# Optimization experiments

Measured on AMD Instinct MI355X. Metric: run time of the kernel, lower is better.

## Reference

```python
import jax, jax.numpy as jnp
import numpy as np

K = 15  # window_size


def setup_inputs() -> dict:
    key = jax.random.key(0)
    k1, k2, k3, k4 = jax.random.split(key, 4)
    x = jax.random.normal(k1, (8, 256, 240, 240), dtype=jnp.float32)
    wq = jax.random.normal(k2, (144, 256), dtype=jnp.float32) * (1.0 / np.sqrt(256))
    wk = jax.random.normal(k3, (144, 256), dtype=jnp.float32) * (1.0 / np.sqrt(256))
    wproj = jax.random.normal(k4, (256, 256), dtype=jnp.float32) * (1.0 / np.sqrt(256))
    return {"x": x, "wq": wq, "wk": wk, "wproj": wproj}


def _pnlm(x, wq, wk, wproj):
    b, c, h, w = x.shape
    ph, pw = (-h) % K, (-w) % K
    if ph or pw:
        x_pad = jnp.pad(x, ((0, 0), (0, 0), (0, ph), (0, pw)), mode='reflect')
    else:
        x_pad = x
    H, W = x_pad.shape[2], x_pad.shape[3]
    nh, nw = H // K, W // K
    N = K * K  # tokens per window
    # blockify: (B,C,H,W) -> (B*nh*nw, C, N)
    blocks = (x_pad.reshape(b, c, nh, K, nw, K)
              .transpose(0, 2, 4, 1, 3, 5)
              .reshape(b * nh * nw, c, N))
    q = jnp.einsum('ec,bcn->bne', wq, blocks)   # (B', N, E)
    km = jnp.einsum('ec,bcm->bem', wk, blocks)  # (B', E, N)
    att = jnp.einsum('bne,bem->bnm', q, km)     # (B', N, N)
    scale = 1.0 / jnp.sqrt(jnp.asarray(q.shape[-1], dtype=att.dtype))
    att = jax.nn.softmax(att * scale, axis=-1)
    y = jnp.einsum('bnm,bcm->bcn', att, blocks)  # att @ V, V = blocks^T
    y = jnp.einsum('oc,bcn->bon', wproj, y)      # 1x1 proj_out
    # unblockify: (B', C, N) -> (B, C, H, W)
    y = (y.reshape(b, nh, nw, c, K, K)
         .transpose(0, 3, 1, 4, 2, 5)
         .reshape(b, c, H, W))
    y = y[:, :, :h, :w]
    return x + y


def reference(x, wq, wk, wproj):
    return _pnlm(x, wq, wk, wproj)
```

## Files before the change

kernel.cpp:

```cpp
#include <hip/hip_runtime.h>


typedef __bf16 bf16x8 __attribute__((ext_vector_type(8)));
typedef float  f32x4  __attribute__((ext_vector_type(4)));

#define MFMA(a,b,c) __builtin_amdgcn_mfma_f32_16x16x32_bf16((a),(b),(c),0,0,0)

#define QK_ROW 320
#define KL_STRIDE 168
#define XBB_ROW 240

__device__ __forceinline__ unsigned short f2bf(float f){
  union { float f; unsigned int u; } v; v.f = f;
  unsigned int r = v.u + 0x7FFFu + ((v.u >> 16) & 1u);
  return (unsigned short)(r >> 16);
}
__device__ __forceinline__ float bf2f(unsigned short u){
  union { unsigned int u; float f; } v; v.u = ((unsigned int)u) << 16;
  return v.f;
}
__device__ __forceinline__ int swz(int row, int col){
  return row*256 + ((((col >> 3) ^ (row & 7)) << 3) | (col & 7));
}
__device__ __forceinline__ bf16x8 ld_frag_lds(const unsigned short* p, int idx){
  uint4 v = *(const uint4*)(p + idx);
  return __builtin_bit_cast(bf16x8, v);
}
__device__ __forceinline__ bf16x8 ld_frag_b(const void* p){
  uint4 v = *(const uint4*)(p);
  return __builtin_bit_cast(bf16x8, v);
}

__device__ __forceinline__ void repack_frag(const unsigned int* plo, const unsigned int* phi,
                                            uint4* outf, int lane){
  const int nn = lane & 15, hh = lane >> 4;
  const int sla = nn + 32*(hh & 1);
  const int slb = sla + 16;
  const bool up = hh >= 2;
  #pragma unroll
  for (int k = 0; k < 8; ++k){
    unsigned int a0 = (unsigned int)__shfl((int)plo[2*k],   sla);
    unsigned int a1 = (unsigned int)__shfl((int)plo[2*k+1], sla);
    unsigned int b0 = (unsigned int)__shfl((int)phi[2*k],   sla);
    unsigned int b1 = (unsigned int)__shfl((int)phi[2*k+1], sla);
    unsigned int c0 = (unsigned int)__shfl((int)plo[2*k],   slb);
    unsigned int c1 = (unsigned int)__shfl((int)plo[2*k+1], slb);
    unsigned int d0 = (unsigned int)__shfl((int)phi[2*k],   slb);
    unsigned int d1 = (unsigned int)__shfl((int)phi[2*k+1], slb);
    outf[k] = make_uint4(up?a1:a0, up?b1:b0, up?c1:c0, up?d1:d0);
  }
}

__global__ __launch_bounds__(256) void k_xb(
    const float* __restrict__ x, unsigned short* __restrict__ xbb)
{
  __shared__ unsigned short xs[8*15*240];
  const int wg = blockIdx.x;
  const int cg = wg & 31;
  const int th = (wg >> 5) & 15;
  const int b  = wg >> 9;
  const int tid = threadIdx.x;

  const float* xb = x + ((size_t)b*256 + cg*8)*57600 + th*15*240;
  for (int i = tid; i < 8*15*120; i += 256){
    int c = i / 1800;
    int rem = i - c*1800;
    int r = rem / 120, p2 = rem - r*120;
    float2 v = *(const float2*)(xb + (size_t)c*57600 + r*240 + p2*2);
    *(unsigned int*)(&xs[(c*15 + r)*240 + p2*2]) =
        (unsigned int)f2bf(v.x) | ((unsigned int)f2bf(v.y) << 16);
  }
  __syncthreads();

  for (int i = tid; i < 8*16*30; i += 256){
    int c = i / 480;
    int rem = i - c*480;
    int tw = rem / 30, ch = rem - tw*30;
    union { unsigned short u16[8]; uint4 u4; } pk;
    #pragma unroll
    for (int j = 0; j < 8; ++j){
      int m = ch*8 + j;
      int r = m / 15, s = m - r*15;
      pk.u16[j] = (m <= 224) ? xs[(c*15 + r)*240 + tw*15 + s] : (unsigned short)0;
    }
    *(uint4*)(xbb + ((size_t)(b*256 + th*16 + tw)*256 + cg*8 + c)*XBB_ROW + ch*8) = pk.u4;
  }
}

__global__ __launch_bounds__(512) void k_qk(
    const float* __restrict__ x, const float* __restrict__ wq,
    const float* __restrict__ wk,
    unsigned short* __restrict__ qkws)
{
  __shared__ __align__(16) unsigned short S[32768];
  unsigned short* xt  = S;
  unsigned short* wqs = S;
  unsigned short* wks = S + 8192;
  const int wg  = blockIdx.x;
  const int b   = wg / 450;
  const int hw0 = (wg % 450) * 128;
  const int tid = threadIdx.x;
  const int lane = tid & 63, wave = tid >> 6;
  const int col  = lane & 15, hi = lane >> 4;

  {
    const float* xb = x + (size_t)b * 256 * 57600 + hw0;
    const int hw_l = tid & 127;
    #pragma unroll 4
    for (int i = 0; i < 32; ++i){
      int c = ((tid >> 7) * 32 + i) * 2;
      float f0 = xb[(size_t)c     * 57600 + hw_l];
      float f1 = xb[(size_t)(c+1) * 57600 + hw_l];
      *(unsigned int*)(&xt[swz(hw_l, c)]) =
          (unsigned int)f2bf(f0) | ((unsigned int)f2bf(f1) << 16);
    }
  }
  __syncthreads();

  bf16x8 af[8];
  const int arow = wave*16 + col;
  #pragma unroll
  for (int k = 0; k < 8; ++k)
    af[k] = ld_frag_lds(xt, swz(arow, k*32 + hi*8));

  const size_t orow_base = (size_t)b*57600 + hw0 + wave*16;

  for (int eg = 0; eg < 5; ++eg){
    __syncthreads();
    for (int i = 0; i < 8; ++i){
      int idx = tid + i*512;
      int e_l = idx >> 7, c = (idx & 127) * 2;
      int e = eg*32 + e_l;
      float2 vq = make_float2(0.f,0.f), vk = make_float2(0.f,0.f);
      if (e < 144){
        vq = *(const float2*)(wq + (size_t)e*256 + c);
        vk = *(const float2*)(wk + (size_t)e*256 + c);
      }
      *(unsigned int*)(&wqs[swz(e_l, c)]) =
          (unsigned int)f2bf(vq.x) | ((unsigned int)f2bf(vq.y) << 16);
      *(unsigned int*)(&wks[swz(e_l, c)]) =
          (unsigned int)f2bf(vk.x) | ((unsigned int)f2bf(vk.y) << 16);
    }
    __syncthreads();
    #pragma unroll
    for (int etl = 0; etl < 2; ++etl){
      f32x4 aq = {0.f,0.f,0.f,0.f}, ak = {0.f,0.f,0.f,0.f};
      const int el = etl*16 + col;
      #pragma unroll
      for (int k = 0; k < 8; ++k){
        int idx = swz(el, k*32 + hi*8);
        bf16x8 bq = ld_frag_lds(wqs, idx);
        bf16x8 bk = ld_frag_lds(wks, idx);
        aq = MFMA(af[k], bq, aq);
        ak = MFMA(af[k], bk, ak);
      }
      const int e_out = eg*32 + etl*16 + col;
      #pragma unroll
      for (int jj = 0; jj < 4; ++jj){
        size_t row = orow_base + hi*4 + jj;
        qkws[row*QK_ROW + e_out]       = f2bf(aq[jj]);
        qkws[row*QK_ROW + 160 + e_out] = f2bf(ak[jj]);
      }
    }
  }
}

__global__ __launch_bounds__(512,4) void k_attn_b(
    const unsigned short* __restrict__ xbb, const float* __restrict__ wproj,
    const unsigned short* __restrict__ qkws, float* __restrict__ out)
{
  __shared__ __align__(16) unsigned short S[40320 + 480];
  unsigned short* kl = S;
  unsigned short* xl = S;
  unsigned short* wl = S + 32768;
  unsigned int*  hwp = (unsigned int*)(S + 40320);
  const int wg = blockIdx.x;
  const int b  = wg >> 8;
  const int th = (wg >> 4) & 15, tw = wg & 15;
  const int h0 = th*15, w0 = tw*15;
  const int tid = threadIdx.x;
  const int lane = tid & 63, wave = tid >> 6;
  const int col  = lane & 15, hi = lane >> 4;
  const size_t obase = (size_t)b * 256 * 57600;
  const unsigned short* qkb = qkws + (size_t)b * 57600 * QK_ROW;
  const unsigned short* xbw = xbb + (size_t)wg * (256*XBB_ROW);

  if (tid < 240){
    int ms = tid <= 224 ? tid : 224;
    hwp[tid] = (unsigned int)((h0 + ms/15)*240 + w0 + ms%15);
  }
  __syncthreads();

  for (int i = tid; i < 240*20; i += 512){
    int m = i / 20, eb = i - m*20;
    *(uint4*)(&kl[m*KL_STRIDE + eb*8]) =
        *(const uint4*)(qkb + (size_t)hwp[m]*QK_ROW + 160 + eb*8);
  }
  __syncthreads();

  uint4 attf[2][8];
  #pragma unroll
  for (int slot = 0; slot < 2; ++slot){
    const int nt = wave + slot*8;
    if (nt < 15){
      const int n  = nt*16 + col;
      const int na = n <= 224 ? n : 224;
      const unsigned short* qrow = qkb + (size_t)hwp[na]*QK_ROW;
      bf16x8 qf[5];
      #pragma unroll
      for (int c = 0; c < 5; ++c)
        qf[c] = ld_frag_b(qrow + c*32 + hi*8);
      f32x4 at[15];
      #pragma unroll
      for (int T = 0; T < 15; ++T){
        f32x4 acc = {0.f,0.f,0.f,0.f};
        #pragma unroll
        for (int c = 0; c < 5; ++c){
          bf16x8 kf = ld_frag_lds(kl, (T*16 + col)*KL_STRIDE + c*32 + hi*8);
          acc = MFMA(kf, qf[c], acc);
        }
        at[T] = acc;
      }
      const float sc = 0.12022458674074695f;
      float M = -3.0e38f;
      #pragma unroll
      for (int T = 0; T < 15; ++T){
        #pragma unroll
        for (int jj = 0; jj < 4; ++jj){
          int m = T*16 + hi*4 + jj;
          if (m <= 224) M = fmaxf(M, at[T][jj]*sc);
        }
      }
      M = fmaxf(M, __shfl_xor(M, 16));
      M = fmaxf(M, __shfl_xor(M, 32));
      float Ssum = 0.f;
      #pragma unroll
      for (int T = 0; T < 15; ++T){
        #pragma unroll
        for (int jj = 0; jj < 4; ++jj){
          int m = T*16 + hi*4 + jj;
          float v = (m <= 224) ? exp2f(at[T][jj]*sc - M) : 0.f;
          at[T][jj] = v; Ssum += v;
        }
      }
      Ssum += __shfl_xor(Ssum, 16);
      Ssum += __shfl_xor(Ssum, 32);
      const float inv = 1.0f / Ssum;
      unsigned int plo[16], phi[16];
      #pragma unroll
      for (int T = 0; T < 15; ++T){
        plo[T] = (unsigned int)f2bf(at[T][0]*inv) | ((unsigned int)f2bf(at[T][1]*inv) << 16);
        phi[T] = (unsigned int)f2bf(at[T][2]*inv) | ((unsigned int)f2bf(at[T][3]*inv) << 16);
      }
      plo[15] = 0u; phi[15] = 0u;
      repack_frag(plo, phi, attf[slot], lane);
    }
  }

  unsigned int ylo[2][16], yhi[2][16];
  #pragma unroll
  for (int half = 0; half < 2; ++half){
    __syncthreads();
    for (int i = tid; i < 128*32; i += 512){
      int c = i >> 5, m8 = i & 31;
      uint4 v = make_uint4(0u,0u,0u,0u);
      if (m8 < 30)
        v = *(const uint4*)(xbw + (size_t)(half*128 + c)*XBB_ROW + m8*8);
      *(uint4*)(&xl[swz(c, m8*8)]) = v;
    }
    __syncthreads();
    #pragma unroll
    for (int slot = 0; slot < 2; ++slot){
      const int nt = wave + slot*8;
      if (nt < 15){
        #pragma unroll
        for (int ct = 0; ct < 8; ++ct){
          f32x4 acc = {0.f,0.f,0.f,0.f};
          #pragma unroll
          for (int k = 0; k < 8; ++k){
            bf16x8 xf = ld_frag_lds(xl, swz(ct*16 + col, k*32 + hi*8));
            acc = MFMA(xf, __builtin_bit_cast(bf16x8, attf[slot][k]), acc);
          }
          ylo[slot][half*8 + ct] = (unsigned int)f2bf(acc[0]) | ((unsigned int)f2bf(acc[1]) << 16);
          yhi[slot][half*8 + ct] = (unsigned int)f2bf(acc[2]) | ((unsigned int)f2bf(acc[3]) << 16);
        }
      }
    }
  }

  uint4 y1f[2][8];
  #pragma unroll
  for (int slot = 0; slot < 2; ++slot){
    const int nt = wave + slot*8;
    if (nt < 15)
      repack_frag(ylo[slot], yhi[slot], y1f[slot], lane);
  }

  #pragma unroll 1
  for (int oe = 0; oe < 16; ++oe){
    __syncthreads();
    for (int i = tid; i < 16*128; i += 512){
      int olr = i >> 7, c = (i & 127)*2;
      const float* wr = wproj + (size_t)(oe*16 + olr)*256 + c;
      *(unsigned int*)(&wl[swz(olr, c)]) =
          (unsigned int)f2bf(wr[0]) | ((unsigned int)f2bf(wr[1]) << 16);
    }
    __syncthreads();
    bf16x8 awf[8];
    #pragma unroll
    for (int k = 0; k < 8; ++k)
      awf[k] = ld_frag_lds(wl, swz(col, k*32 + hi*8));
    #pragma unroll
    for (int slot = 0; slot < 2; ++slot){
      const int nt = wave + slot*8;
      if (nt < 15){
        f32x4 y2 = {0.f,0.f,0.f,0.f};
        #pragma unroll
        for (int k = 0; k < 8; ++k)
          y2 = MFMA(awf[k], __builtin_bit_cast(bf16x8, y1f[slot][k]), y2);
        const int n = nt*16 + col;
        if (n <= 224){
          const size_t pix = hwp[n];
          #pragma unroll
          for (int jj = 0; jj < 4; ++jj){
            int o = oe*16 + hi*4 + jj;
            float xr = bf2f(xbw[(size_t)o*XBB_ROW + n]);
            out[obase + (size_t)o*57600 + pix] = y2[jj] + xr;
          }
        }
      }
    }
  }
}

__global__ __launch_bounds__(512,4) void k_attn_s(
    const float* __restrict__ x, const float* __restrict__ wproj,
    const unsigned short* __restrict__ qkws, float* __restrict__ out)
{
  __shared__ __align__(16) unsigned short S[40320 + 480];
  unsigned short* kl = S;
  unsigned short* xl = S;
  unsigned short* wl = S + 32768;
  unsigned int*  hwp = (unsigned int*)(S + 40320);
  const int wg = blockIdx.x;
  const int b  = wg >> 8;
  const int th = (wg >> 4) & 15, tw = wg & 15;
  const int h0 = th*15, w0 = tw*15;
  const int tid = threadIdx.x;
  const int lane = tid & 63, wave = tid >> 6;
  const int col  = lane & 15, hi = lane >> 4;
  const size_t xbase = (size_t)b * 256 * 57600;
  const unsigned short* qkb = qkws + (size_t)b * 57600 * QK_ROW;

  if (tid < 240){
    int ms = tid <= 224 ? tid : 224;
    hwp[tid] = (unsigned int)((h0 + ms/15)*240 + w0 + ms%15);
  }
  __syncthreads();

  for (int i = tid; i < 240*20; i += 512){
    int m = i / 20, eb = i - m*20;
    *(uint4*)(&kl[m*KL_STRIDE + eb*8]) =
        *(const uint4*)(qkb + (size_t)hwp[m]*QK_ROW + 160 + eb*8);
  }
  __syncthreads();

  uint4 attf[2][8];
  #pragma unroll
  for (int slot = 0; slot < 2; ++slot){
    const int nt = wave + slot*8;
    if (nt < 15){
      const int n  = nt*16 + col;
      const int na = n <= 224 ? n : 224;
      const unsigned short* qrow = qkb + (size_t)hwp[na]*QK_ROW;
      bf16x8 qf[5];
      #pragma unroll
      for (int c = 0; c < 5; ++c)
        qf[c] = ld_frag_b(qrow + c*32 + hi*8);
      f32x4 at[15];
      #pragma unroll
      for (int T = 0; T < 15; ++T){
        f32x4 acc = {0.f,0.f,0.f,0.f};
        #pragma unroll
        for (int c = 0; c < 5; ++c){
          bf16x8 kf = ld_frag_lds(kl, (T*16 + col)*KL_STRIDE + c*32 + hi*8);
          acc = MFMA(kf, qf[c], acc);
        }
        at[T] = acc;
      }
      const float sc = 0.12022458674074695f;
      float M = -3.0e38f;
      #pragma unroll
      for (int T = 0; T < 15; ++T){
        #pragma unroll
        for (int jj = 0; jj < 4; ++jj){
          int m = T*16 + hi*4 + jj;
          if (m <= 224) M = fmaxf(M, at[T][jj]*sc);
        }
      }
      M = fmaxf(M, __shfl_xor(M, 16));
      M = fmaxf(M, __shfl_xor(M, 32));
      float Ssum = 0.f;
      #pragma unroll
      for (int T = 0; T < 15; ++T){
        #pragma unroll
        for (int jj = 0; jj < 4; ++jj){
          int m = T*16 + hi*4 + jj;
          float v = (m <= 224) ? exp2f(at[T][jj]*sc - M) : 0.f;
          at[T][jj] = v; Ssum += v;
        }
      }
      Ssum += __shfl_xor(Ssum, 16);
      Ssum += __shfl_xor(Ssum, 32);
      const float inv = 1.0f / Ssum;
      unsigned int plo[16], phi[16];
      #pragma unroll
      for (int T = 0; T < 15; ++T){
        plo[T] = (unsigned int)f2bf(at[T][0]*inv) | ((unsigned int)f2bf(at[T][1]*inv) << 16);
        phi[T] = (unsigned int)f2bf(at[T][2]*inv) | ((unsigned int)f2bf(at[T][3]*inv) << 16);
      }
      plo[15] = 0u; phi[15] = 0u;
      repack_frag(plo, phi, attf[slot], lane);
    }
  }

  unsigned int ylo[2][16], yhi[2][16];
  #pragma unroll
  for (int half = 0; half < 2; ++half){
    __syncthreads();
    for (int i = tid; i < 128*128; i += 512){
      int c = i >> 7, m = (i & 127)*2;
      int m0 = m <= 224 ? m : 224;
      float f0 = (m     <= 224) ? x[xbase + (size_t)(half*128 + c)*57600 + hwp[m0]]   : 0.f;
      float f1 = (m + 1 <= 224) ? x[xbase + (size_t)(half*128 + c)*57600 + hwp[m0+1]] : 0.f;
      *(unsigned int*)(&xl[swz(c, m)]) =
          (unsigned int)f2bf(f0) | ((unsigned int)f2bf(f1) << 16);
    }
    __syncthreads();
    #pragma unroll
    for (int slot = 0; slot < 2; ++slot){
      const int nt = wave + slot*8;
      if (nt < 15){
        #pragma unroll
        for (int ct = 0; ct < 8; ++ct){
          f32x4 acc = {0.f,0.f,0.f,0.f};
          #pragma unroll
          for (int k = 0; k < 8; ++k){
            bf16x8 xf = ld_frag_lds(xl, swz(ct*16 + col, k*32 + hi*8));
            acc = MFMA(xf, __builtin_bit_cast(bf16x8, attf[slot][k]), acc);
          }
          ylo[slot][half*8 + ct] = (unsigned int)f2bf(acc[0]) | ((unsigned int)f2bf(acc[1]) << 16);
          yhi[slot][half*8 + ct] = (unsigned int)f2bf(acc[2]) | ((unsigned int)f2bf(acc[3]) << 16);
        }
      }
    }
  }

  uint4 y1f[2][8];
  #pragma unroll
  for (int slot = 0; slot < 2; ++slot){
    const int nt = wave + slot*8;
    if (nt < 15)
      repack_frag(ylo[slot], yhi[slot], y1f[slot], lane);
  }

  #pragma unroll 1
  for (int oe = 0; oe < 16; ++oe){
    __syncthreads();
    for (int i = tid; i < 16*128; i += 512){
      int olr = i >> 7, c = (i & 127)*2;
      const float* wr = wproj + (size_t)(oe*16 + olr)*256 + c;
      *(unsigned int*)(&wl[swz(olr, c)]) =
          (unsigned int)f2bf(wr[0]) | ((unsigned int)f2bf(wr[1]) << 16);
    }
    __syncthreads();
    bf16x8 awf[8];
    #pragma unroll
    for (int k = 0; k < 8; ++k)
      awf[k] = ld_frag_lds(wl, swz(col, k*32 + hi*8));
    #pragma unroll
    for (int slot = 0; slot < 2; ++slot){
      const int nt = wave + slot*8;
      if (nt < 15){
        f32x4 y2 = {0.f,0.f,0.f,0.f};
        #pragma unroll
        for (int k = 0; k < 8; ++k)
          y2 = MFMA(awf[k], __builtin_bit_cast(bf16x8, y1f[slot][k]), y2);
        const int n = nt*16 + col;
        if (n <= 224){
          const size_t pix = hwp[n];
          #pragma unroll
          for (int jj = 0; jj < 4; ++jj){
            int o = oe*16 + hi*4 + jj;
            const size_t idx = xbase + (size_t)o*57600 + pix;
            out[idx] = y2[jj] + x[idx];
          }
        }
      }
    }
  }
}

extern "C" void kernel_launch(void* const* d_in, const int* in_sizes, int n_in,
                              void* d_out, int out_size, void* d_ws, size_t ws_size,
                              hipStream_t stream)
{
  const float* x     = (const float*)d_in[0];
  const float* wq    = (const float*)d_in[1];
  const float* wk    = (const float*)d_in[2];
  const float* wproj = (const float*)d_in[3];
  float* out = (float*)d_out;
  (void)in_sizes; (void)n_in; (void)out_size;

  const size_t QKWS_B = (size_t)8*57600*QK_ROW*2;
  const size_t XBB_B  = (size_t)8*256*256*XBB_ROW*2;
  unsigned short* qkws = (unsigned short*)d_ws;

  if (ws_size >= QKWS_B + XBB_B){
    unsigned short* xbb = (unsigned short*)((char*)d_ws + QKWS_B);
    k_xb    <<<dim3(4096), dim3(256), 0, stream>>>(x, xbb);
    k_qk    <<<dim3(3600), dim3(512), 0, stream>>>(x, wq, wk, qkws);
    k_attn_b<<<dim3(2048), dim3(512), 0, stream>>>(xbb, wproj, qkws, out);
  } else {
    k_qk    <<<dim3(3600), dim3(512), 0, stream>>>(x, wq, wk, qkws);
    k_attn_s<<<dim3(2048), dim3(512), 0, stream>>>(x, wproj, qkws, out);
  }
}
```

Before: 1.083 ms.

## Compute Q/K projection from pre-blockified bf16 x and pre-converted bf16 weights

```diff
diff --git a/kernel.cpp b/kernel.cpp
--- a/kernel.cpp
+++ b/kernel.cpp
@@ -21,6 +21,9 @@
 }
 __device__ __forceinline__ int swz(int row, int col){
   return row*256 + ((((col >> 3) ^ (row & 7)) << 3) | (col & 7));
+}
+__device__ __forceinline__ int swzC(int row, int col){
+  return row*256 + (col ^ ((((row >> 3) ^ row) & 7) << 3));
 }
 __device__ __forceinline__ bf16x8 ld_frag_lds(const unsigned short* p, int idx){
   uint4 v = *(const uint4*)(p + idx);
@@ -51,6 +54,32 @@
   }
 }
 
+__global__ __launch_bounds__(256) void k_w(
+    const float* __restrict__ wq, const float* __restrict__ wk,
+    const float* __restrict__ wproj,
+    unsigned short* __restrict__ wqb, unsigned short* __restrict__ wkb,
+    unsigned short* __restrict__ wpb)
+{
+  int i = blockIdx.x*256 + threadIdx.x;
+  if (i < 20480){
+    int e = i >> 7, c = (i & 127)*2;
+    unsigned int v = 0;
+    if (e < 144) v = (unsigned int)f2bf(wq[e*256+c]) | ((unsigned int)f2bf(wq[e*256+c+1]) << 16);
+    *(unsigned int*)(wqb + (size_t)i*2) = v;
+  } else if (i < 40960){
+    int j = i - 20480;
+    int e = j >> 7, c = (j & 127)*2;
+    unsigned int v = 0;
+    if (e < 144) v = (unsigned int)f2bf(wk[e*256+c]) | ((unsigned int)f2bf(wk[e*256+c+1]) << 16);
+    *(unsigned int*)(wkb + (size_t)j*2) = v;
+  } else if (i < 73728){
+    int l = i - 40960;
+    int o = l >> 7, c = (l & 127)*2;
+    *(unsigned int*)(wpb + (size_t)l*2) =
+        (unsigned int)f2bf(wproj[o*256+c]) | ((unsigned int)f2bf(wproj[o*256+c+1]) << 16);
+  }
+}
+
 __global__ __launch_bounds__(256) void k_xb(
     const float* __restrict__ x, unsigned short* __restrict__ xbb)
 {
@@ -84,6 +113,91 @@
       pk.u16[j] = (m <= 224) ? xs[(c*15 + r)*240 + tw*15 + s] : (unsigned short)0;
     }
     *(uint4*)(xbb + ((size_t)(b*256 + th*16 + tw)*256 + cg*8 + c)*XBB_ROW + ch*8) = pk.u4;
+  }
+}
+
+__global__ __launch_bounds__(512) void k_qkb(
+    const unsigned short* __restrict__ xbb,
+    const unsigned short* __restrict__ wqb, const unsigned short* __restrict__ wkb,
+    unsigned short* __restrict__ qkws)
+{
+  __shared__ __align__(16) unsigned short S[32768];
+  unsigned short* xt  = S;
+  unsigned short* wqs = S;
+  unsigned short* wks = S + 8192;
+  const int wg = blockIdx.x;
+  const int b  = wg >> 8;
+  const int th = (wg >> 4) & 15, tw = wg & 15;
+  const int h0 = th*15, w0 = tw*15;
+  const int tid = threadIdx.x;
+  const int lane = tid & 63, wave = tid >> 6;
+  const int col  = lane & 15, hi = lane >> 4;
+  const unsigned short* xbw = xbb + (size_t)wg * (256*XBB_ROW);
+
+  #pragma unroll 1
+  for (int half = 0; half < 2; ++half){
+    if (half) __syncthreads();
+    for (int i = tid; i < 256*16; i += 512){
+      int c = i >> 4, m8 = i & 15;
+      int m = half*128 + m8*8;
+      if (m < 240){
+        uint4 v = *(const uint4*)(xbw + (size_t)c*XBB_ROW + m);
+        const unsigned short* pv = (const unsigned short*)&v;
+        #pragma unroll
+        for (int j = 0; j < 8; ++j)
+          xt[swzC(m8*8 + j, c)] = pv[j];
+      }
+    }
+    __syncthreads();
+
+    const int t = half*8 + wave;
+    const bool act = t < 15;
+    bf16x8 af[8];
+    if (act){
+      const int rloc = wave*16 + col;
+      #pragma unroll
+      for (int k = 0; k < 8; ++k)
+        af[k] = ld_frag_lds(xt, swzC(rloc, k*32 + hi*8));
+    }
+    __syncthreads();
+
+    #pragma unroll 1
+    for (int eg = 0; eg < 5; ++eg){
+      if (eg) __syncthreads();
+      for (int i = tid; i < 32*32; i += 512){
+        int e_l = i >> 5, c8 = (i & 31)*8;
+        size_t off = (size_t)(eg*32 + e_l)*256 + c8;
+        *(uint4*)(&wqs[swz(e_l, c8)]) = *(const uint4*)(wqb + off);
+        *(uint4*)(&wks[swz(e_l, c8)]) = *(const uint4*)(wkb + off);
+      }
+      __syncthreads();
+      if (act){
+        #pragma unroll
+        for (int et = 0; et < 2; ++et){
+          f32x4 aq = {0.f,0.f,0.f,0.f}, ak = {0.f,0.f,0.f,0.f};
+          const int el = et*16 + col;
+          #pragma unroll
+          for (int k = 0; k < 8; ++k){
+            int idx = swz(el, k*32 + hi*8);
+            bf16x8 bq = ld_frag_lds(wqs, idx);
+            bf16x8 bk = ld_frag_lds(wks, idx);
+            aq = MFMA(af[k], bq, aq);
+            ak = MFMA(af[k], bk, ak);
+          }
+          const int e_out = eg*32 + et*16 + col;
+          #pragma unroll
+          for (int jj = 0; jj < 4; ++jj){
+            int m_px = t*16 + hi*4 + jj;
+            if (m_px <= 224){
+              int hw = (h0 + m_px/15)*240 + w0 + m_px%15;
+              size_t row = ((size_t)b*57600 + hw)*QK_ROW;
+              qkws[row + e_out]       = f2bf(aq[jj]);
+              qkws[row + 160 + e_out] = f2bf(ak[jj]);
+            }
+          }
+        }
+      }
+    }
   }
 }
 
@@ -514,9 +628,21 @@
 
   const size_t QKWS_B = (size_t)8*57600*QK_ROW*2;
   const size_t XBB_B  = (size_t)8*256*256*XBB_ROW*2;
+  const size_t WQB_B  = (size_t)160*256*2;
+  const size_t WKB_B  = (size_t)160*256*2;
+  const size_t WPB_B  = (size_t)256*256*2;
   unsigned short* qkws = (unsigned short*)d_ws;
 
-  if (ws_size >= QKWS_B + XBB_B){
+  if (ws_size >= QKWS_B + XBB_B + WQB_B + WKB_B + WPB_B){
+    unsigned short* xbb = (unsigned short*)((char*)d_ws + QKWS_B);
+    unsigned short* wqb = (unsigned short*)((char*)d_ws + QKWS_B + XBB_B);
+    unsigned short* wkb = wqb + 160*256;
+    unsigned short* wpb = wkb + 160*256;
+    k_w     <<<dim3(288),  dim3(256), 0, stream>>>(wq, wk, wproj, wqb, wkb, wpb);
+    k_xb    <<<dim3(4096), dim3(256), 0, stream>>>(x, xbb);
+    k_qkb   <<<dim3(2048), dim3(512), 0, stream>>>(xbb, wqb, wkb, qkws);
+    k_attn_b<<<dim3(2048), dim3(512), 0, stream>>>(xbb, wproj, qkws, out);
+  } else if (ws_size >= QKWS_B + XBB_B){
     unsigned short* xbb = (unsigned short*)((char*)d_ws + QKWS_B);
     k_xb    <<<dim3(4096), dim3(256), 0, stream>>>(x, xbb);
     k_qk    <<<dim3(3600), dim3(512), 0, stream>>>(x, wq, wk, qkws);
```

Result: faster. 1.040 ms (-4.0%).
